# Kernel optimization log

Hardware: AMD Instinct MI355X
Metric: run time of the kernel (lower is better)

Reference implementation:

```python
import jax, jax.numpy as jnp
import numpy as np

D_MODEL = 1024
NUM_TILES = 64
TPC = 8                      # tiles_per_cluster
NUM_CLUSTERS = NUM_TILES // TPC
GRID = 16
COMP_H = 256                 # compress hidden = d_model // 4
NUM_KNOTS = 8
EPS_LN = 1e-5


def setup_inputs() -> dict:
    key = jax.random.key(0)
    ks = jax.random.split(key, 12)
    B, T = 4, 4096
    x = jax.random.normal(ks[0], (B, T, D_MODEL), dtype=jnp.float32)
    signatures_raw = jax.random.normal(ks[1], (NUM_TILES, D_MODEL), dtype=jnp.float32) * 0.5
    knot_values = jax.nn.sigmoid(jnp.linspace(-3.0, 3.0, NUM_KNOTS).astype(jnp.float32))
    temperature = jnp.ones((1,), dtype=jnp.float32)
    # compress: Linear(d,comp_h) -> GELU -> Linear(comp_h,2) -> Tanh
    compress_w1 = jax.random.normal(ks[2], (D_MODEL, COMP_H), dtype=jnp.float32) * (1.0 / np.sqrt(D_MODEL))
    compress_b1 = jnp.zeros((COMP_H,), dtype=jnp.float32)
    compress_w2 = jax.random.normal(ks[3], (COMP_H, 2), dtype=jnp.float32) * (1.0 / np.sqrt(COMP_H))
    compress_b2 = jnp.zeros((2,), dtype=jnp.float32)
    # per-tile magnitude splines: Linear(2,grid) -> ReLU -> Linear(grid,1)
    spline_w1 = jax.random.normal(ks[4], (NUM_TILES, 2, GRID), dtype=jnp.float32) * (1.0 / np.sqrt(2.0))
    spline_b1 = jnp.zeros((NUM_TILES, GRID), dtype=jnp.float32)
    spline_w2 = jax.random.normal(ks[5], (NUM_TILES, GRID, 1), dtype=jnp.float32) * (1.0 / np.sqrt(GRID))
    spline_b2 = jnp.zeros((NUM_TILES, 1), dtype=jnp.float32)
    directions = jax.random.normal(ks[6], (NUM_TILES, D_MODEL), dtype=jnp.float32) * 0.02
    norm_gamma = jnp.ones((D_MODEL,), dtype=jnp.float32)
    norm_beta = jnp.zeros((D_MODEL,), dtype=jnp.float32)
    output_scale = jnp.ones((1,), dtype=jnp.float32) * 0.1
    return dict(x=x, signatures_raw=signatures_raw, knot_values=knot_values,
                temperature=temperature, compress_w1=compress_w1, compress_b1=compress_b1,
                compress_w2=compress_w2, compress_b2=compress_b2, spline_w1=spline_w1,
                spline_b1=spline_b1, spline_w2=spline_w2, spline_b2=spline_b2,
                directions=directions, norm_gamma=norm_gamma, norm_beta=norm_beta,
                output_scale=output_scale)


def _calibrate(scores, knots, temperature):
    # ScoreCalibrationSpline: sigmoid -> linear interpolation over knots
    K = knots.shape[0]
    normalized = jax.nn.sigmoid(scores / (temperature[0] + 1e-6))
    idx_float = normalized * (K - 1)
    idx_low = jnp.clip(idx_float.astype(jnp.int32), 0, K - 2)
    idx_high = idx_low + 1
    t = idx_float - idx_low.astype(scores.dtype)
    val_low = knots[idx_low]
    val_high = knots[idx_high]
    return val_low + t * (val_high - val_low)


def _forward(x, signatures_raw, knot_values, temperature, compress_w1, compress_b1,
             compress_w2, compress_b2, spline_w1, spline_b1, spline_w2, spline_b2,
             directions, norm_gamma, norm_beta, output_scale):
    B, T, D = x.shape
    xf = x.reshape(-1, D)  # [N, D]

    # ternary quantized signatures with straight-through estimator
    q = jnp.where(signatures_raw > 0.3, 1.0,
                  jnp.where(signatures_raw < -0.3, -1.0, 0.0)).astype(signatures_raw.dtype)
    sigs = signatures_raw + jax.lax.stop_gradient(q - signatures_raw)  # [NT, D]

    # hierarchical routing: cluster signatures = sign(mean of member sigs)
    cluster_sigs = jnp.sign(sigs.reshape(NUM_CLUSTERS, TPC, D).mean(axis=1))  # [NC, D]
    cluster_scores = xf @ cluster_sigs.T                                       # [N, NC]
    cluster_gates = _calibrate(cluster_scores, knot_values, temperature)
    cluster_idx = jnp.argmax(cluster_gates, axis=-1)                           # [N]

    # within-cluster tile selection (clusters are contiguous blocks of tiles)
    tile_scores = xf @ sigs.T                                                  # [N, NT]
    tile_gates = _calibrate(tile_scores, knot_values, temperature)
    gates_by_cluster = tile_gates.reshape(-1, NUM_CLUSTERS, TPC)
    sel_gates = jnp.take_along_axis(gates_by_cluster, cluster_idx[:, None, None],
                                    axis=1)[:, 0, :]                            # [N, TPC]
    local_idx = jnp.argmax(sel_gates, axis=-1)
    tile_idx = cluster_idx * TPC + local_idx                                    # [N]

    # compress to 2D spline coordinates
    h = jax.nn.gelu(xf @ compress_w1 + compress_b1, approximate=False)
    comp = jnp.tanh(h @ compress_w2 + compress_b2)                              # [N, 2]

    # batched per-token tiny spline MLP (gather selected tile's weights)
    w1 = spline_w1[tile_idx]                                                    # [N, 2, G]
    b1 = spline_b1[tile_idx]                                                    # [N, G]
    hh = jax.nn.relu(jnp.einsum('ni,nig->ng', comp, w1) + b1)                   # [N, G]
    w2 = spline_w2[tile_idx]                                                    # [N, G, 1]
    b2 = spline_b2[tile_idx]                                                    # [N, 1]
    mag = jnp.einsum('ng,ngo->no', hh, w2) + b2                                 # [N, 1]

    ffn_out = mag * directions[tile_idx] * output_scale[0]                      # [N, D]

    # residual + LayerNorm (dropout in eval mode = identity)
    y = xf + ffn_out
    mu = y.mean(axis=-1, keepdims=True)
    var = ((y - mu) ** 2).mean(axis=-1, keepdims=True)
    y = (y - mu) / jnp.sqrt(var + EPS_LN) * norm_gamma + norm_beta
    return y.reshape(B, T, D)


def reference(x, signatures_raw, knot_values, temperature, compress_w1, compress_b1,
              compress_w2, compress_b2, spline_w1, spline_b1, spline_w2, spline_b2,
              directions, norm_gamma, norm_beta, output_scale):
    return _forward(x, signatures_raw, knot_values, temperature, compress_w1, compress_b1,
                    compress_w2, compress_b2, spline_w1, spline_b1, spline_w2, spline_b2,
                    directions, norm_gamma, norm_beta, output_scale)
```

## Files before the change

kernel.cpp:

```cpp
#include <hip/hip_runtime.h>
#include <hip/hip_bf16.h>
#include <cmath>

#define N_TOK 16384
#define DM    1024
#define CH    256
#define SGRID 16
#define NB    352
#define NSC   72
#define CHUNKS_PER_KT 2816
#define KT_BYTES      45056
#define KT_USHORT     22528

typedef __attribute__((ext_vector_type(8))) short short8;
typedef __attribute__((ext_vector_type(4))) float floatx4;

__device__ __forceinline__ unsigned short f2bf(float f) {
  union { float f; unsigned int u; } v; v.f = f;
  unsigned int r = v.u + 0x7FFFu + ((v.u >> 16) & 1u);
  return (unsigned short)(r >> 16);
}

__device__ __forceinline__ float calibrate(float s, const float* __restrict__ kn, float temp_eff) {
  float nrm = 1.0f / (1.0f + expf(-s / temp_eff));
  float idxf = nrm * 7.0f;
  int il = (int)idxf; if (il > 6) il = 6;
  float tt = idxf - (float)il;
  float lo = kn[il], hi = kn[il + 1];
  return lo + tt * (hi - lo);
}

__global__ __launch_bounds__(256) void prep_kernel(
    const float* __restrict__ sig_raw, const float* __restrict__ w1,
    unsigned short* __restrict__ wsB) {
  int bid = blockIdx.x, tid = threadIdx.x;
  if (bid < 64) {
    __shared__ float tile[64 * 68];
    int ng = bid & 3, kt = bid >> 2;
    int r = tid >> 2, cb = (tid & 3) * 16;
    const float* src = w1 + (size_t)(kt * 64 + r) * CH + ng * 64 + cb;
#pragma unroll
    for (int i = 0; i < 4; ++i)
      *(float4*)(tile + r * 68 + cb + 4 * i) = *(const float4*)(src + 4 * i);
    __syncthreads();
#pragma unroll
    for (int h = 0; h < 2; ++h) {
      int cl = h * 256 + tid;
      int ntl = cl >> 7, rest = cl & 127;
      int ks = rest >> 6, quad = (rest >> 4) & 3, l15 = rest & 15;
      int nl = ntl * 16 + l15;
      int kl = ks * 32 + quad * 8;
      short8 v;
#pragma unroll
      for (int j = 0; j < 8; ++j) v[j] = (short)f2bf(tile[(kl + j) * 68 + nl]);
      int c = (ng * 4 + ntl) * 128 + rest;
      *(short8*)(wsB + (size_t)kt * KT_USHORT + c * 8) = v;
    }
  } else {
    int g = (bid - 64) * 256 + tid;
    int kt = g / 768, rem = g % 768;
    int ntl = rem >> 7, rest = rem & 127;
    int nt = 16 + ntl;
    int ks = rest >> 6, quad = (rest >> 4) & 3, l15 = rest & 15;
    int n = nt * 16 + l15;
    int k0 = kt * 64 + ks * 32 + quad * 8;
    short8 v;
#pragma unroll
    for (int j = 0; j < 8; ++j) {
      int k = k0 + j;
      unsigned short bv = 0;
      if (n < 264) {
        int cl2 = n - 256;
        float s = 0.f;
#pragma unroll
        for (int m = 0; m < 8; ++m) {
          float rr = sig_raw[(size_t)(cl2 * 8 + m) * DM + k];
          s += (rr > 0.3f) ? 1.f : ((rr < -0.3f) ? -1.f : 0.f);
        }
        bv = (s > 0.f) ? 0x3F80u : ((s < 0.f) ? 0xBF80u : 0u);
      } else if (n < 328) {
        float rr = sig_raw[(size_t)(n - 264) * DM + k];
        bv = (rr > 0.3f) ? 0x3F80u : ((rr < -0.3f) ? 0xBF80u : 0u);
      }
      v[j] = (short)bv;
    }
    *(short8*)(wsB + (size_t)kt * KT_USHORT + (nt * 128 + rest) * 8) = v;
  }
}

__global__ __launch_bounds__(256, 2) void gemm_kernel(
    const float* __restrict__ x, const unsigned short* __restrict__ wsB,
    const float* __restrict__ b1, const float* __restrict__ w2,
    const float* __restrict__ b2, float* __restrict__ comp_out,
    float* __restrict__ score_ws) {
  __shared__ unsigned short Ash[64 * 72];
  __shared__ unsigned short Bsh[KT_USHORT];
  __shared__ float Psh[4][64][2];

  int tid = threadIdx.x;
  int wave = tid >> 6, lane = tid & 63, quad = lane >> 4, l15 = lane & 15;
  int m0 = blockIdx.x * 64;

  floatx4 acc[6][4];
#pragma unroll
  for (int s = 0; s < 6; ++s)
#pragma unroll
    for (int mt = 0; mt < 4; ++mt) acc[s][mt] = (floatx4){0.f, 0.f, 0.f, 0.f};

  int arow = tid >> 2, akk = (tid & 3) * 16;
  const float* asrc = x + (size_t)(m0 + arow) * DM + akk;

  for (int kt = 0; kt < 16; ++kt) {
    __syncthreads();
    {
      const char* gB = (const char*)wsB + (size_t)kt * KT_BYTES;
      char* lB = (char*)Bsh;
#pragma unroll
      for (int i = 0; i < 11; ++i) {
        int off = (i * 4 + wave) * 1024;
        __builtin_amdgcn_global_load_lds(
            (const __attribute__((address_space(1))) void*)(gB + off + lane * 16),
            (__attribute__((address_space(3))) void*)(lB + off), 16, 0, 0);
      }
    }
    {
      const float* s = asrc + kt * 64;
      float4 f0 = ((const float4*)s)[0], f1 = ((const float4*)s)[1];
      float4 f2 = ((const float4*)s)[2], f3 = ((const float4*)s)[3];
      short8 v0, v1;
      v0[0] = (short)f2bf(f0.x); v0[1] = (short)f2bf(f0.y);
      v0[2] = (short)f2bf(f0.z); v0[3] = (short)f2bf(f0.w);
      v0[4] = (short)f2bf(f1.x); v0[5] = (short)f2bf(f1.y);
      v0[6] = (short)f2bf(f1.z); v0[7] = (short)f2bf(f1.w);
      v1[0] = (short)f2bf(f2.x); v1[1] = (short)f2bf(f2.y);
      v1[2] = (short)f2bf(f2.z); v1[3] = (short)f2bf(f2.w);
      v1[4] = (short)f2bf(f3.x); v1[5] = (short)f2bf(f3.y);
      v1[6] = (short)f2bf(f3.z); v1[7] = (short)f2bf(f3.w);
      *(short8*)(Ash + arow * 72 + akk) = v0;
      *(short8*)(Ash + arow * 72 + akk + 8) = v1;
    }
    __syncthreads();
#pragma unroll
    for (int ks = 0; ks < 2; ++ks) {
      short8 a[4];
#pragma unroll
      for (int mt = 0; mt < 4; ++mt)
        a[mt] = *(const short8*)(Ash + (mt * 16 + l15) * 72 + ks * 32 + quad * 8);
#pragma unroll
      for (int s = 0; s < 5; ++s) {
        int nt = wave + s * 4;
        short8 b = *(const short8*)(Bsh + (nt * 128 + ks * 64 + quad * 16 + l15) * 8);
#pragma unroll
        for (int mt = 0; mt < 4; ++mt)
          acc[s][mt] = __builtin_amdgcn_mfma_f32_16x16x32_bf16(a[mt], b, acc[s][mt], 0, 0, 0);
      }
      if (wave == 0) {
        short8 b = *(const short8*)(Bsh + (20 * 128 + ks * 64 + quad * 16 + l15) * 8);
#pragma unroll
        for (int mt = 0; mt < 4; ++mt)
          acc[5][mt] = __builtin_amdgcn_mfma_f32_16x16x32_bf16(a[mt], b, acc[5][mt], 0, 0, 0);
      }
    }
  }

  float p0[4][4], p1[4][4];
#pragma unroll
  for (int mt = 0; mt < 4; ++mt)
#pragma unroll
    for (int r = 0; r < 4; ++r) { p0[mt][r] = 0.f; p1[mt][r] = 0.f; }
#pragma unroll
  for (int s = 0; s < 4; ++s) {
    int col = (wave + s * 4) * 16 + l15;
    float b1c = b1[col], w20 = w2[2 * col], w21 = w2[2 * col + 1];
#pragma unroll
    for (int mt = 0; mt < 4; ++mt)
#pragma unroll
      for (int r = 0; r < 4; ++r) {
        float h = acc[s][mt][r] + b1c;
        h = 0.5f * h * (1.0f + erff(h * 0.7071067811865475f));
        p0[mt][r] += h * w20;
        p1[mt][r] += h * w21;
      }
  }
#pragma unroll
  for (int m = 1; m < 16; m <<= 1)
#pragma unroll
    for (int mt = 0; mt < 4; ++mt)
#pragma unroll
      for (int r = 0; r < 4; ++r) {
        p0[mt][r] += __shfl_xor(p0[mt][r], m);
        p1[mt][r] += __shfl_xor(p1[mt][r], m);
      }
  if (l15 == 0) {
#pragma unroll
    for (int mt = 0; mt < 4; ++mt)
#pragma unroll
      for (int r = 0; r < 4; ++r) {
        Psh[wave][mt * 16 + quad * 4 + r][0] = p0[mt][r];
        Psh[wave][mt * 16 + quad * 4 + r][1] = p1[mt][r];
      }
  }
  {
    int cs = wave * 16 + l15;
#pragma unroll
    for (int mt = 0; mt < 4; ++mt)
#pragma unroll
      for (int r = 0; r < 4; ++r)
        score_ws[(size_t)(m0 + mt * 16 + quad * 4 + r) * NSC + cs] = acc[4][mt][r];
    if (wave == 0 && l15 < 8) {
#pragma unroll
      for (int mt = 0; mt < 4; ++mt)
#pragma unroll
        for (int r = 0; r < 4; ++r)
          score_ws[(size_t)(m0 + mt * 16 + quad * 4 + r) * NSC + 64 + l15] = acc[5][mt][r];
    }
  }
  __syncthreads();
  if (tid < 64) {
    float s0 = b2[0], s1 = b2[1];
#pragma unroll
    for (int w = 0; w < 4; ++w) { s0 += Psh[w][tid][0]; s1 += Psh[w][tid][1]; }
    comp_out[(m0 + tid) * 2 + 0] = tanhf(s0);
    comp_out[(m0 + tid) * 2 + 1] = tanhf(s1);
  }
}

__global__ __launch_bounds__(256) void finalize_kernel(
    const float* __restrict__ x, const float* __restrict__ score_ws,
    const float* __restrict__ knots, const float* __restrict__ temperature,
    const float* __restrict__ comp_ws, const float* __restrict__ sw1,
    const float* __restrict__ sb1, const float* __restrict__ sw2,
    const float* __restrict__ sb2, const float* __restrict__ dirs,
    const float* __restrict__ gma, const float* __restrict__ bta,
    const float* __restrict__ oscale, float* __restrict__ out) {
  int tid = threadIdx.x;
  int wave = tid >> 6, lane = tid & 63;
  int tok = blockIdx.x * 4 + wave;
  const float* xr = x + (size_t)tok * DM;
  float4 xv[4];
#pragma unroll
  for (int i = 0; i < 4; ++i) xv[i] = *(const float4*)(xr + 4 * lane + 256 * i);

  float temp_eff = temperature[0] + 1e-6f;
  const float* sc = score_ws + (size_t)tok * NSC;

  int cid = 0; float best = -1e30f;
#pragma unroll
  for (int c = 0; c < 8; ++c) {
    float g = calibrate(sc[c], knots, temp_eff);
    if (g > best) { best = g; cid = c; }
  }
  int lidx = 0; best = -1e30f;
#pragma unroll
  for (int j = 0; j < 8; ++j) {
    float g = calibrate(sc[8 + cid * 8 + j], knots, temp_eff);
    if (g > best) { best = g; lidx = j; }
  }
  int t = cid * 8 + lidx;

  float c0 = comp_ws[tok * 2], c1 = comp_ws[tok * 2 + 1];
  float mag = sb2[t];
#pragma unroll
  for (int g2 = 0; g2 < SGRID; ++g2) {
    float hh = c0 * sw1[t * 32 + g2] + c1 * sw1[t * 32 + 16 + g2] + sb1[t * 16 + g2];
    hh = fmaxf(hh, 0.f);
    mag += hh * sw2[t * 16 + g2];
  }
  float scale = mag * oscale[0];

  const float* dr = dirs + (size_t)t * DM;
  float4 fv[4];
  float ssum = 0.f;
#pragma unroll
  for (int i = 0; i < 4; ++i) {
    float4 d4 = *(const float4*)(dr + 4 * lane + 256 * i);
    fv[i].x = xv[i].x + scale * d4.x;
    fv[i].y = xv[i].y + scale * d4.y;
    fv[i].z = xv[i].z + scale * d4.z;
    fv[i].w = xv[i].w + scale * d4.w;
    ssum += fv[i].x + fv[i].y + fv[i].z + fv[i].w;
  }
#pragma unroll
  for (int m = 1; m < 64; m <<= 1) ssum += __shfl_xor(ssum, m);
  float mu = ssum * (1.0f / 1024.0f);
  float vs = 0.f;
#pragma unroll
  for (int i = 0; i < 4; ++i) {
    float d0 = fv[i].x - mu, d1 = fv[i].y - mu, d2 = fv[i].z - mu, d3 = fv[i].w - mu;
    vs += d0 * d0 + d1 * d1 + d2 * d2 + d3 * d3;
  }
#pragma unroll
  for (int m = 1; m < 64; m <<= 1) vs += __shfl_xor(vs, m);
  float inv = rsqrtf(vs * (1.0f / 1024.0f) + 1e-5f);

  float* orow = out + (size_t)tok * DM;
#pragma unroll
  for (int i = 0; i < 4; ++i) {
    float4 g4 = *(const float4*)(gma + 4 * lane + 256 * i);
    float4 b4 = *(const float4*)(bta + 4 * lane + 256 * i);
    float4 o;
    o.x = (fv[i].x - mu) * inv * g4.x + b4.x;
    o.y = (fv[i].y - mu) * inv * g4.y + b4.y;
    o.z = (fv[i].z - mu) * inv * g4.z + b4.z;
    o.w = (fv[i].w - mu) * inv * g4.w + b4.w;
    *(float4*)(orow + 4 * lane + 256 * i) = o;
  }
}

extern "C" void kernel_launch(void* const* d_in, const int* in_sizes, int n_in,
                              void* d_out, int out_size, void* d_ws, size_t ws_size,
                              hipStream_t stream) {
  const float* x      = (const float*)d_in[0];
  const float* sigraw = (const float*)d_in[1];
  const float* knots  = (const float*)d_in[2];
  const float* temp   = (const float*)d_in[3];
  const float* cw1    = (const float*)d_in[4];
  const float* cb1    = (const float*)d_in[5];
  const float* cw2    = (const float*)d_in[6];
  const float* cb2    = (const float*)d_in[7];
  const float* sw1    = (const float*)d_in[8];
  const float* sb1    = (const float*)d_in[9];
  const float* sw2    = (const float*)d_in[10];
  const float* sb2    = (const float*)d_in[11];
  const float* dirs   = (const float*)d_in[12];
  const float* gma    = (const float*)d_in[13];
  const float* bta    = (const float*)d_in[14];
  const float* oscale = (const float*)d_in[15];
  float* out = (float*)d_out;

  char* ws = (char*)d_ws;
  unsigned short* wsB = (unsigned short*)ws;
  float* score_ws     = (float*)(ws + 720896);
  float* comp         = (float*)(ws + 720896 + 4718592);

  hipLaunchKernelGGL(prep_kernel, dim3(112), dim3(256), 0, stream,
                     sigraw, cw1, wsB);
  hipLaunchKernelGGL(gemm_kernel, dim3(N_TOK / 64), dim3(256), 0, stream,
                     x, wsB, cb1, cw2, cb2, comp, score_ws);
  hipLaunchKernelGGL(finalize_kernel, dim3(N_TOK / 4), dim3(256), 0, stream,
                     x, score_ws, knots, temp, comp,
                     sw1, sb1, sw2, sb2, dirs, gma, bta, oscale, out);
}
```

Before: 199.8 us.

## Fuse GEMM and finalize into one kernel with register-direct MFMA operand loads

Merges the compress/score GEMM and the routing/LayerNorm finalize into a single 512-thread kernel. Scores and compress outputs stay in shared memory instead of round-tripping through workspace. The GEMM now loads B fragments and fp32 A rows straight into registers from a repacked per-32-K layout, with a two-stage software prefetch and no LDS staging or barriers in the K loop. The prep kernel is rewritten to compute that layout, and LayerNorm uses a single-pass sum/sum-of-squares. The fused kernel re-reads x rows for the epilogue, hoping for cache hits, and the one-pass variance may lose some precision.

```diff
diff --git a/kernel.cpp b/kernel.cpp
--- a/kernel.cpp
+++ b/kernel.cpp
@@ -6,11 +6,7 @@
 #define DM    1024
 #define CH    256
 #define SGRID 16
-#define NB    352
-#define NSC   72
-#define CHUNKS_PER_KT 2816
-#define KT_BYTES      45056
-#define KT_USHORT     22528
+#define NTP   24
 
 typedef __attribute__((ext_vector_type(8))) short short8;
 typedef __attribute__((ext_vector_type(4))) float floatx4;
@@ -19,6 +15,15 @@
   union { float f; unsigned int u; } v; v.f = f;
   unsigned int r = v.u + 0x7FFFu + ((v.u >> 16) & 1u);
   return (unsigned short)(r >> 16);
+}
+
+__device__ __forceinline__ short8 cvt8(float4 u, float4 v) {
+  union { short8 s; __hip_bfloat162 h[4]; } r;
+  r.h[0] = __float22bfloat162_rn(make_float2(u.x, u.y));
+  r.h[1] = __float22bfloat162_rn(make_float2(u.z, u.w));
+  r.h[2] = __float22bfloat162_rn(make_float2(v.x, v.y));
+  r.h[3] = __float22bfloat162_rn(make_float2(v.z, v.w));
+  return r.s;
 }
 
 __device__ __forceinline__ float calibrate(float s, const float* __restrict__ kn, float temp_eff) {
@@ -33,277 +38,258 @@
 __global__ __launch_bounds__(256) void prep_kernel(
     const float* __restrict__ sig_raw, const float* __restrict__ w1,
     unsigned short* __restrict__ wsB) {
-  int bid = blockIdx.x, tid = threadIdx.x;
-  if (bid < 64) {
-    __shared__ float tile[64 * 68];
-    int ng = bid & 3, kt = bid >> 2;
-    int r = tid >> 2, cb = (tid & 3) * 16;
-    const float* src = w1 + (size_t)(kt * 64 + r) * CH + ng * 64 + cb;
-#pragma unroll
-    for (int i = 0; i < 4; ++i)
-      *(float4*)(tile + r * 68 + cb + 4 * i) = *(const float4*)(src + 4 * i);
-    __syncthreads();
-#pragma unroll
-    for (int h = 0; h < 2; ++h) {
-      int cl = h * 256 + tid;
-      int ntl = cl >> 7, rest = cl & 127;
-      int ks = rest >> 6, quad = (rest >> 4) & 3, l15 = rest & 15;
-      int nl = ntl * 16 + l15;
-      int kl = ks * 32 + quad * 8;
+  __shared__ float Wt[32][260];
+  __shared__ float St[64][33];
+  int kk = blockIdx.x, tid = threadIdx.x;
+  {
+    int r = tid >> 3, c0 = (tid & 7) * 32;
+    const float* src = w1 + (size_t)(kk * 32 + r) * CH + c0;
+#pragma unroll
+    for (int i = 0; i < 8; ++i)
+      *(float4*)(&Wt[r][c0 + 4 * i]) = *(const float4*)(src + 4 * i);
+  }
+  {
+    int t = tid >> 2, c0 = (tid & 3) * 8;
+    const float* src = sig_raw + (size_t)t * DM + kk * 32 + c0;
+#pragma unroll
+    for (int i = 0; i < 8; ++i) {
+      float rr = src[i];
+      St[t][c0 + i] = (rr > 0.3f) ? 1.f : ((rr < -0.3f) ? -1.f : 0.f);
+    }
+  }
+  __syncthreads();
+#pragma unroll
+  for (int i = 0; i < 4; ++i) {
+    int idx = i * 256 + tid;
+    int nt = idx >> 6, lane = idx & 63;
+    int q = lane >> 4, l = lane & 15;
+    short8 v;
+#pragma unroll
+    for (int j = 0; j < 8; ++j) v[j] = (short)f2bf(Wt[q * 8 + j][nt * 16 + l]);
+    *(short8*)(wsB + ((size_t)(kk * NTP + nt) * 64 + lane) * 8) = v;
+  }
+#pragma unroll
+  for (int i = 0; i < 2; ++i) {
+    int idx = i * 256 + tid;
+    if (idx < 320) {
+      int nt = 16 + (idx >> 6), lane = idx & 63;
+      int q = lane >> 4, l = lane & 15;
+      int n = nt * 16 + l;
       short8 v;
 #pragma unroll
-      for (int j = 0; j < 8; ++j) v[j] = (short)f2bf(tile[(kl + j) * 68 + nl]);
-      int c = (ng * 4 + ntl) * 128 + rest;
-      *(short8*)(wsB + (size_t)kt * KT_USHORT + c * 8) = v;
-    }
-  } else {
-    int g = (bid - 64) * 256 + tid;
-    int kt = g / 768, rem = g % 768;
-    int ntl = rem >> 7, rest = rem & 127;
-    int nt = 16 + ntl;
-    int ks = rest >> 6, quad = (rest >> 4) & 3, l15 = rest & 15;
-    int n = nt * 16 + l15;
-    int k0 = kt * 64 + ks * 32 + quad * 8;
-    short8 v;
-#pragma unroll
-    for (int j = 0; j < 8; ++j) {
-      int k = k0 + j;
-      unsigned short bv = 0;
-      if (n < 264) {
-        int cl2 = n - 256;
-        float s = 0.f;
-#pragma unroll
-        for (int m = 0; m < 8; ++m) {
-          float rr = sig_raw[(size_t)(cl2 * 8 + m) * DM + k];
-          s += (rr > 0.3f) ? 1.f : ((rr < -0.3f) ? -1.f : 0.f);
+      for (int j = 0; j < 8; ++j) {
+        int kl = q * 8 + j;
+        float val = 0.f;
+        if (n < 264) {
+          float s = 0.f;
+#pragma unroll
+          for (int m = 0; m < 8; ++m) s += St[(n - 256) * 8 + m][kl];
+          val = (s > 0.f) ? 1.f : ((s < 0.f) ? -1.f : 0.f);
+        } else if (n < 328) {
+          val = St[n - 264][kl];
         }
-        bv = (s > 0.f) ? 0x3F80u : ((s < 0.f) ? 0xBF80u : 0u);
-      } else if (n < 328) {
-        float rr = sig_raw[(size_t)(n - 264) * DM + k];
-        bv = (rr > 0.3f) ? 0x3F80u : ((rr < -0.3f) ? 0xBF80u : 0u);
+        v[j] = (short)f2bf(val);
       }
-      v[j] = (short)bv;
-    }
-    *(short8*)(wsB + (size_t)kt * KT_USHORT + (nt * 128 + rest) * 8) = v;
-  }
-}
-
-__global__ __launch_bounds__(256, 2) void gemm_kernel(
+      *(short8*)(wsB + ((size_t)(kk * NTP + nt) * 64 + lane) * 8) = v;
+    }
+  }
+}
+
+#define LOADK(kk, bv, av)                                                   \
+  {                                                                         \
+    const char* bp = bBase + (size_t)(kk) * (NTP * 1024);                   \
+    _Pragma("unroll") for (int s = 0; s < 6; ++s)                           \
+        bv[s] = *(const short8*)(bp + s * 4096);                            \
+    const float* ap0 = aBase0 + (kk) * 32;                                  \
+    av[0][0] = *(const float4*)(ap0);                                       \
+    av[0][1] = *(const float4*)(ap0 + 4);                                   \
+    const float* ap1 = aBase1 + (kk) * 32;                                  \
+    av[1][0] = *(const float4*)(ap1);                                       \
+    av[1][1] = *(const float4*)(ap1 + 4);                                   \
+  }
+
+#define COMPUTE(bv, av)                                                     \
+  {                                                                         \
+    short8 aa0 = cvt8(av[0][0], av[0][1]);                                  \
+    short8 aa1 = cvt8(av[1][0], av[1][1]);                                  \
+    _Pragma("unroll") for (int s = 0; s < 6; ++s) {                         \
+      acc[s][0] = __builtin_amdgcn_mfma_f32_16x16x32_bf16(aa0, bv[s], acc[s][0], 0, 0, 0); \
+      acc[s][1] = __builtin_amdgcn_mfma_f32_16x16x32_bf16(aa1, bv[s], acc[s][1], 0, 0, 0); \
+    }                                                                       \
+  }
+
+__global__ __launch_bounds__(512, 2) void fused_kernel(
     const float* __restrict__ x, const unsigned short* __restrict__ wsB,
     const float* __restrict__ b1, const float* __restrict__ w2,
-    const float* __restrict__ b2, float* __restrict__ comp_out,
-    float* __restrict__ score_ws) {
-  __shared__ unsigned short Ash[64 * 72];
-  __shared__ unsigned short Bsh[KT_USHORT];
-  __shared__ float Psh[4][64][2];
-
-  int tid = threadIdx.x;
-  int wave = tid >> 6, lane = tid & 63, quad = lane >> 4, l15 = lane & 15;
-  int m0 = blockIdx.x * 64;
-
-  floatx4 acc[6][4];
-#pragma unroll
-  for (int s = 0; s < 6; ++s)
-#pragma unroll
-    for (int mt = 0; mt < 4; ++mt) acc[s][mt] = (floatx4){0.f, 0.f, 0.f, 0.f};
-
-  int arow = tid >> 2, akk = (tid & 3) * 16;
-  const float* asrc = x + (size_t)(m0 + arow) * DM + akk;
-
-  for (int kt = 0; kt < 16; ++kt) {
-    __syncthreads();
-    {
-      const char* gB = (const char*)wsB + (size_t)kt * KT_BYTES;
-      char* lB = (char*)Bsh;
-#pragma unroll
-      for (int i = 0; i < 11; ++i) {
-        int off = (i * 4 + wave) * 1024;
-        __builtin_amdgcn_global_load_lds(
-            (const __attribute__((address_space(1))) void*)(gB + off + lane * 16),
-            (__attribute__((address_space(3))) void*)(lB + off), 16, 0, 0);
-      }
-    }
-    {
-      const float* s = asrc + kt * 64;
-      float4 f0 = ((const float4*)s)[0], f1 = ((const float4*)s)[1];
-      float4 f2 = ((const float4*)s)[2], f3 = ((const float4*)s)[3];
-      short8 v0, v1;
-      v0[0] = (short)f2bf(f0.x); v0[1] = (short)f2bf(f0.y);
-      v0[2] = (short)f2bf(f0.z); v0[3] = (short)f2bf(f0.w);
-      v0[4] = (short)f2bf(f1.x); v0[5] = (short)f2bf(f1.y);
-      v0[6] = (short)f2bf(f1.z); v0[7] = (short)f2bf(f1.w);
-      v1[0] = (short)f2bf(f2.x); v1[1] = (short)f2bf(f2.y);
-      v1[2] = (short)f2bf(f2.z); v1[3] = (short)f2bf(f2.w);
-      v1[4] = (short)f2bf(f3.x); v1[5] = (short)f2bf(f3.y);
-      v1[6] = (short)f2bf(f3.z); v1[7] = (short)f2bf(f3.w);
-      *(short8*)(Ash + arow * 72 + akk) = v0;
-      *(short8*)(Ash + arow * 72 + akk + 8) = v1;
-    }
-    __syncthreads();
-#pragma unroll
-    for (int ks = 0; ks < 2; ++ks) {
-      short8 a[4];
-#pragma unroll
-      for (int mt = 0; mt < 4; ++mt)
-        a[mt] = *(const short8*)(Ash + (mt * 16 + l15) * 72 + ks * 32 + quad * 8);
-#pragma unroll
-      for (int s = 0; s < 5; ++s) {
-        int nt = wave + s * 4;
-        short8 b = *(const short8*)(Bsh + (nt * 128 + ks * 64 + quad * 16 + l15) * 8);
-#pragma unroll
-        for (int mt = 0; mt < 4; ++mt)
-          acc[s][mt] = __builtin_amdgcn_mfma_f32_16x16x32_bf16(a[mt], b, acc[s][mt], 0, 0, 0);
-      }
-      if (wave == 0) {
-        short8 b = *(const short8*)(Bsh + (20 * 128 + ks * 64 + quad * 16 + l15) * 8);
-#pragma unroll
-        for (int mt = 0; mt < 4; ++mt)
-          acc[5][mt] = __builtin_amdgcn_mfma_f32_16x16x32_bf16(a[mt], b, acc[5][mt], 0, 0, 0);
-      }
-    }
-  }
-
-  float p0[4][4], p1[4][4];
-#pragma unroll
-  for (int mt = 0; mt < 4; ++mt)
-#pragma unroll
-    for (int r = 0; r < 4; ++r) { p0[mt][r] = 0.f; p1[mt][r] = 0.f; }
-#pragma unroll
-  for (int s = 0; s < 4; ++s) {
-    int col = (wave + s * 4) * 16 + l15;
-    float b1c = b1[col], w20 = w2[2 * col], w21 = w2[2 * col + 1];
-#pragma unroll
-    for (int mt = 0; mt < 4; ++mt)
-#pragma unroll
-      for (int r = 0; r < 4; ++r) {
-        float h = acc[s][mt][r] + b1c;
-        h = 0.5f * h * (1.0f + erff(h * 0.7071067811865475f));
-        p0[mt][r] += h * w20;
-        p1[mt][r] += h * w21;
-      }
-  }
-#pragma unroll
-  for (int m = 1; m < 16; m <<= 1)
-#pragma unroll
-    for (int mt = 0; mt < 4; ++mt)
-#pragma unroll
-      for (int r = 0; r < 4; ++r) {
-        p0[mt][r] += __shfl_xor(p0[mt][r], m);
-        p1[mt][r] += __shfl_xor(p1[mt][r], m);
-      }
-  if (l15 == 0) {
-#pragma unroll
-    for (int mt = 0; mt < 4; ++mt)
-#pragma unroll
-      for (int r = 0; r < 4; ++r) {
-        Psh[wave][mt * 16 + quad * 4 + r][0] = p0[mt][r];
-        Psh[wave][mt * 16 + quad * 4 + r][1] = p1[mt][r];
-      }
-  }
-  {
-    int cs = wave * 16 + l15;
-#pragma unroll
-    for (int mt = 0; mt < 4; ++mt)
-#pragma unroll
-      for (int r = 0; r < 4; ++r)
-        score_ws[(size_t)(m0 + mt * 16 + quad * 4 + r) * NSC + cs] = acc[4][mt][r];
-    if (wave == 0 && l15 < 8) {
-#pragma unroll
-      for (int mt = 0; mt < 4; ++mt)
-#pragma unroll
-        for (int r = 0; r < 4; ++r)
-          score_ws[(size_t)(m0 + mt * 16 + quad * 4 + r) * NSC + 64 + l15] = acc[5][mt][r];
-    }
-  }
-  __syncthreads();
-  if (tid < 64) {
-    float s0 = b2[0], s1 = b2[1];
-#pragma unroll
-    for (int w = 0; w < 4; ++w) { s0 += Psh[w][tid][0]; s1 += Psh[w][tid][1]; }
-    comp_out[(m0 + tid) * 2 + 0] = tanhf(s0);
-    comp_out[(m0 + tid) * 2 + 1] = tanhf(s1);
-  }
-}
-
-__global__ __launch_bounds__(256) void finalize_kernel(
-    const float* __restrict__ x, const float* __restrict__ score_ws,
-    const float* __restrict__ knots, const float* __restrict__ temperature,
-    const float* __restrict__ comp_ws, const float* __restrict__ sw1,
+    const float* __restrict__ b2, const float* __restrict__ knots,
+    const float* __restrict__ temperature, const float* __restrict__ sw1,
     const float* __restrict__ sb1, const float* __restrict__ sw2,
     const float* __restrict__ sb2, const float* __restrict__ dirs,
     const float* __restrict__ gma, const float* __restrict__ bta,
     const float* __restrict__ oscale, float* __restrict__ out) {
+  __shared__ float Ssc[64][81];
+  __shared__ float Psh[8][32][3];
+  __shared__ float ScaleS[64];
+  __shared__ int   TidxS[64];
+
   int tid = threadIdx.x;
-  int wave = tid >> 6, lane = tid & 63;
-  int tok = blockIdx.x * 4 + wave;
-  const float* xr = x + (size_t)tok * DM;
-  float4 xv[4];
-#pragma unroll
-  for (int i = 0; i < 4; ++i) xv[i] = *(const float4*)(xr + 4 * lane + 256 * i);
-
-  float temp_eff = temperature[0] + 1e-6f;
-  const float* sc = score_ws + (size_t)tok * NSC;
-
-  int cid = 0; float best = -1e30f;
-#pragma unroll
-  for (int c = 0; c < 8; ++c) {
-    float g = calibrate(sc[c], knots, temp_eff);
-    if (g > best) { best = g; cid = c; }
-  }
-  int lidx = 0; best = -1e30f;
-#pragma unroll
-  for (int j = 0; j < 8; ++j) {
-    float g = calibrate(sc[8 + cid * 8 + j], knots, temp_eff);
-    if (g > best) { best = g; lidx = j; }
-  }
-  int t = cid * 8 + lidx;
-
-  float c0 = comp_ws[tok * 2], c1 = comp_ws[tok * 2 + 1];
-  float mag = sb2[t];
-#pragma unroll
-  for (int g2 = 0; g2 < SGRID; ++g2) {
-    float hh = c0 * sw1[t * 32 + g2] + c1 * sw1[t * 32 + 16 + g2] + sb1[t * 16 + g2];
-    hh = fmaxf(hh, 0.f);
-    mag += hh * sw2[t * 16 + g2];
-  }
-  float scale = mag * oscale[0];
-
-  const float* dr = dirs + (size_t)t * DM;
-  float4 fv[4];
-  float ssum = 0.f;
+  int wave = tid >> 6, lane = tid & 63, quad = lane >> 4, l15 = lane & 15;
+  int w3 = wave & 3, h = wave >> 2;
+  int m0 = blockIdx.x * 64;
+
+  floatx4 acc[6][2];
+#pragma unroll
+  for (int s = 0; s < 6; ++s) {
+    acc[s][0] = (floatx4){0.f, 0.f, 0.f, 0.f};
+    acc[s][1] = (floatx4){0.f, 0.f, 0.f, 0.f};
+  }
+
+  const char* bBase = (const char*)wsB + w3 * 1024 + lane * 16;
+  const float* aBase0 = x + (size_t)(m0 + h * 32 + l15) * DM + quad * 8;
+  const float* aBase1 = aBase0 + 16 * DM;
+
+  short8 bA[6], bB_[6];
+  float4 aA[2][2], aB_[2][2];
+  LOADK(0, bA, aA);
+#pragma unroll 1
+  for (int kk = 0; kk < 30; kk += 2) {
+    LOADK(kk + 1, bB_, aB_);
+    COMPUTE(bA, aA);
+    LOADK(kk + 2, bA, aA);
+    COMPUTE(bB_, aB_);
+  }
+  LOADK(31, bB_, aB_);
+  COMPUTE(bA, aA);
+  COMPUTE(bB_, aB_);
+
+#pragma unroll
+  for (int mt2 = 0; mt2 < 2; ++mt2)
+#pragma unroll
+    for (int r = 0; r < 4; ++r) {
+      int row = h * 32 + mt2 * 16 + quad * 4 + r;
+      Ssc[row][w3 * 16 + l15] = acc[4][mt2][r];
+      if (w3 == 0) Ssc[row][64 + l15] = acc[5][mt2][r];
+    }
+
+  float p0[2][4], p1[2][4];
+#pragma unroll
+  for (int mt2 = 0; mt2 < 2; ++mt2)
+#pragma unroll
+    for (int r = 0; r < 4; ++r) { p0[mt2][r] = 0.f; p1[mt2][r] = 0.f; }
+#pragma unroll
+  for (int s = 0; s < 4; ++s) {
+    int col = (w3 + 4 * s) * 16 + l15;
+    float b1c = b1[col], w20 = w2[2 * col], w21 = w2[2 * col + 1];
+#pragma unroll
+    for (int mt2 = 0; mt2 < 2; ++mt2)
+#pragma unroll
+      for (int r = 0; r < 4; ++r) {
+        float hh = acc[s][mt2][r] + b1c;
+        hh = 0.5f * hh * (1.0f + erff(hh * 0.7071067811865475f));
+        p0[mt2][r] += hh * w20;
+        p1[mt2][r] += hh * w21;
+      }
+  }
+#pragma unroll
+  for (int m = 1; m < 16; m <<= 1)
+#pragma unroll
+    for (int mt2 = 0; mt2 < 2; ++mt2)
+#pragma unroll
+      for (int r = 0; r < 4; ++r) {
+        p0[mt2][r] += __shfl_xor(p0[mt2][r], m);
+        p1[mt2][r] += __shfl_xor(p1[mt2][r], m);
+      }
+  if (l15 == 0) {
+#pragma unroll
+    for (int mt2 = 0; mt2 < 2; ++mt2)
+#pragma unroll
+      for (int r = 0; r < 4; ++r) {
+        Psh[wave][mt2 * 16 + quad * 4 + r][0] = p0[mt2][r];
+        Psh[wave][mt2 * 16 + quad * 4 + r][1] = p1[mt2][r];
+      }
+  }
+  __syncthreads();
+
+  if (tid < 64) {
+    int row = tid, hh2 = row >> 5, rl = row & 31;
+    float s0 = b2[0], s1 = b2[1];
+#pragma unroll
+    for (int j = 0; j < 4; ++j) {
+      s0 += Psh[hh2 * 4 + j][rl][0];
+      s1 += Psh[hh2 * 4 + j][rl][1];
+    }
+    float c0 = tanhf(s0), c1 = tanhf(s1);
+
+    float temp_eff = temperature[0] + 1e-6f;
+    int cid = 0; float best = -1e30f;
+#pragma unroll
+    for (int c = 0; c < 8; ++c) {
+      float g = calibrate(Ssc[row][c], knots, temp_eff);
+      if (g > best) { best = g; cid = c; }
+    }
+    int lidx = 0; best = -1e30f;
+#pragma unroll
+    for (int j = 0; j < 8; ++j) {
+      float g = calibrate(Ssc[row][8 + cid * 8 + j], knots, temp_eff);
+      if (g > best) { best = g; lidx = j; }
+    }
+    int t = cid * 8 + lidx;
+
+    float mag = sb2[t];
+#pragma unroll
+    for (int g2 = 0; g2 < SGRID; ++g2) {
+      float hv = c0 * sw1[t * 32 + g2] + c1 * sw1[t * 32 + 16 + g2] + sb1[t * 16 + g2];
+      hv = fmaxf(hv, 0.f);
+      mag += hv * sw2[t * 16 + g2];
+    }
+    ScaleS[row] = mag * oscale[0];
+    TidxS[row] = t;
+  }
+  __syncthreads();
+
+  float4 g4[4], be4[4];
 #pragma unroll
   for (int i = 0; i < 4; ++i) {
-    float4 d4 = *(const float4*)(dr + 4 * lane + 256 * i);
-    fv[i].x = xv[i].x + scale * d4.x;
-    fv[i].y = xv[i].y + scale * d4.y;
-    fv[i].z = xv[i].z + scale * d4.z;
-    fv[i].w = xv[i].w + scale * d4.w;
-    ssum += fv[i].x + fv[i].y + fv[i].z + fv[i].w;
-  }
-#pragma unroll
-  for (int m = 1; m < 64; m <<= 1) ssum += __shfl_xor(ssum, m);
-  float mu = ssum * (1.0f / 1024.0f);
-  float vs = 0.f;
-#pragma unroll
-  for (int i = 0; i < 4; ++i) {
-    float d0 = fv[i].x - mu, d1 = fv[i].y - mu, d2 = fv[i].z - mu, d3 = fv[i].w - mu;
-    vs += d0 * d0 + d1 * d1 + d2 * d2 + d3 * d3;
-  }
-#pragma unroll
-  for (int m = 1; m < 64; m <<= 1) vs += __shfl_xor(vs, m);
-  float inv = rsqrtf(vs * (1.0f / 1024.0f) + 1e-5f);
-
-  float* orow = out + (size_t)tok * DM;
-#pragma unroll
-  for (int i = 0; i < 4; ++i) {
-    float4 g4 = *(const float4*)(gma + 4 * lane + 256 * i);
-    float4 b4 = *(const float4*)(bta + 4 * lane + 256 * i);
-    float4 o;
-    o.x = (fv[i].x - mu) * inv * g4.x + b4.x;
-    o.y = (fv[i].y - mu) * inv * g4.y + b4.y;
-    o.z = (fv[i].z - mu) * inv * g4.z + b4.z;
-    o.w = (fv[i].w - mu) * inv * g4.w + b4.w;
-    *(float4*)(orow + 4 * lane + 256 * i) = o;
+    g4[i] = *(const float4*)(gma + 4 * lane + 256 * i);
+    be4[i] = *(const float4*)(bta + 4 * lane + 256 * i);
+  }
+#pragma unroll 1
+  for (int rr = 0; rr < 8; ++rr) {
+    int row = wave * 8 + rr;
+    float scale = ScaleS[row];
+    const float* xr = x + (size_t)(m0 + row) * DM;
+    const float* dr = dirs + (size_t)TidxS[row] * DM;
+    float4 fv[4];
+    float ssum = 0.f, ssq = 0.f;
+#pragma unroll
+    for (int i = 0; i < 4; ++i) {
+      float4 xv = *(const float4*)(xr + 4 * lane + 256 * i);
+      float4 d4 = *(const float4*)(dr + 4 * lane + 256 * i);
+      fv[i].x = xv.x + scale * d4.x;
+      fv[i].y = xv.y + scale * d4.y;
+      fv[i].z = xv.z + scale * d4.z;
+      fv[i].w = xv.w + scale * d4.w;
+      ssum += fv[i].x + fv[i].y + fv[i].z + fv[i].w;
+      ssq += fv[i].x * fv[i].x + fv[i].y * fv[i].y + fv[i].z * fv[i].z + fv[i].w * fv[i].w;
+    }
+#pragma unroll
+    for (int m = 1; m < 64; m <<= 1) {
+      ssum += __shfl_xor(ssum, m);
+      ssq += __shfl_xor(ssq, m);
+    }
+    float mu = ssum * (1.0f / 1024.0f);
+    float var = ssq * (1.0f / 1024.0f) - mu * mu;
+    float inv = rsqrtf(var + 1e-5f);
+    float* orow = out + (size_t)(m0 + row) * DM;
+#pragma unroll
+    for (int i = 0; i < 4; ++i) {
+      float4 o;
+      o.x = (fv[i].x - mu) * inv * g4[i].x + be4[i].x;
+      o.y = (fv[i].y - mu) * inv * g4[i].y + be4[i].y;
+      o.z = (fv[i].z - mu) * inv * g4[i].z + be4[i].z;
+      o.w = (fv[i].w - mu) * inv * g4[i].w + be4[i].w;
+      *(float4*)(orow + 4 * lane + 256 * i) = o;
+    }
   }
 }
 
@@ -328,16 +314,11 @@
   const float* oscale = (const float*)d_in[15];
   float* out = (float*)d_out;
 
-  char* ws = (char*)d_ws;
-  unsigned short* wsB = (unsigned short*)ws;
-  float* score_ws     = (float*)(ws + 720896);
-  float* comp         = (float*)(ws + 720896 + 4718592);
-
-  hipLaunchKernelGGL(prep_kernel, dim3(112), dim3(256), 0, stream,
+  unsigned short* wsB = (unsigned short*)d_ws;
+
+  hipLaunchKernelGGL(prep_kernel, dim3(32), dim3(256), 0, stream,
                      sigraw, cw1, wsB);
-  hipLaunchKernelGGL(gemm_kernel, dim3(N_TOK / 64), dim3(256), 0, stream,
-                     x, wsB, cb1, cw2, cb2, comp, score_ws);
-  hipLaunchKernelGGL(finalize_kernel, dim3(N_TOK / 4), dim3(256), 0, stream,
-                     x, score_ws, knots, temp, comp,
+  hipLaunchKernelGGL(fused_kernel, dim3(N_TOK / 64), dim3(512), 0, stream,
+                     x, wsB, cb1, cw2, cb2, knots, temp,
                      sw1, sb1, sw2, sb2, dirs, gma, bta, oscale, out);
 }
```

After: 198.4 us. About the same (-0.7%).
